# Performance work log

Hardware: AMD Instinct MI355X
Metric: run time of the kernel (lower is better)

## Reference

```python
import jax, jax.numpy as jnp
import numpy as np

BG_W = 1.0
DILATED_BG_W = 5.0
EDGE_W = 20.0
KSIZE = 3


def setup_inputs() -> dict:
    key = jax.random.key(0)
    k1, k2 = jax.random.split(key)
    B, C, H, W = 16, 1, 1024, 1024
    pred = jax.random.normal(k1, (B, C, H, W), dtype=jnp.float32)
    target = (jax.random.uniform(k2, (B, C, H, W)) < 0.05).astype(jnp.float32)
    return {"pred": pred, "target": target}


def _dilate(target):
    # cv2.dilate with KSIZExKSIZE rect kernel == max pool, stride 1, SAME padding
    return jax.lax.reduce_window(
        target, -jnp.inf, jax.lax.max,
        window_dimensions=(1, 1, KSIZE, KSIZE),
        window_strides=(1, 1, 1, 1),
        padding="SAME",
    )


def reference(pred, target):
    dilated = _dilate(target)
    # weight: edge pixels (target>0.5) -> EDGE_W, else dilated band -> DILATED_BG_W, else BG_W
    weight = jnp.where(target > 0.5, EDGE_W,
                       jnp.where(dilated > 0.5, DILATED_BG_W, BG_W))
    # binary_cross_entropy_with_logits, reduction='none', then mean
    x = pred
    losses = weight * (jnp.maximum(x, 0.0) - x * target + jnp.log1p(jnp.exp(-jnp.abs(x))))
    return jnp.mean(losses)
```

## Files before the change

kernel.cpp:

```cpp
#include <hip/hip_runtime.h>

#define HH 1024
#define WW 1024
#define BAND 16
#define NT 256

typedef __attribute__((ext_vector_type(4))) float f32x4;

__device__ __forceinline__ float fmax3(float a, float b, float c) {
    return fmaxf(a, fmaxf(b, c));
}

__device__ __forceinline__ float loss_elem(float x, float t, float dil) {
    float w = fmaf(15.0f, t, fmaf(4.0f, dil, 1.0f));
    float a  = fabsf(x);
    float sp = __logf(1.0f + __expf(-a));
    return w * (fmaxf(x, 0.0f) - x * t + sp);
}

template <bool PER_WAVE>
__global__ __launch_bounds__(NT)
__attribute__((amdgpu_waves_per_eu(2, 2)))
void dilatedweightBCE_main(
        const float* __restrict__ pred,
        const float* __restrict__ target,
        float* __restrict__ partial) {
    __shared__ float swave[NT / 64];
    __shared__ float ldsL[NT / 64][BAND];
    __shared__ float ldsR[NT / 64][BAND];

    const int t    = threadIdx.x;
    const int lane = t & 63;
    const int wv   = t >> 6;
    const int c    = t * 4;

    const int l    = blockIdx.x;
    const int xcd  = l & 7;
    const int j    = l >> 3;
    const int img  = j >> 3;
    const int slab = j & 7;
    const int h0   = (xcd * 8 + slab) * BAND;

    const float* timg = target + (size_t)img * HH * WW;
    const float* pimg = pred   + (size_t)img * HH * WW;
    const f32x4 zero = (f32x4)(0.0f);

    f32x4 tr[BAND + 2];
    tr[0] = (h0 > 0)
          ? __builtin_nontemporal_load((const f32x4*)(timg + (size_t)(h0 - 1) * WW + c))
          : zero;
    #pragma unroll
    for (int r = 0; r < BAND; ++r)
        tr[r + 1] = __builtin_nontemporal_load(
            (const f32x4*)(timg + (size_t)(h0 + r) * WW + c));
    tr[BAND + 1] = (h0 + BAND < HH)
          ? __builtin_nontemporal_load((const f32x4*)(timg + (size_t)(h0 + BAND) * WW + c))
          : zero;

    f32x4 xr[BAND];
    #pragma unroll
    for (int r = 0; r < BAND; ++r)
        xr[r] = __builtin_nontemporal_load(
            (const f32x4*)(pimg + (size_t)(h0 + r) * WW + c));

    if (lane == 0) {
        #pragma unroll
        for (int r = 0; r < BAND; ++r)
            ldsL[wv][r] = fmax3(tr[r].x, tr[r + 1].x, tr[r + 2].x);
    }
    if (lane == 63) {
        #pragma unroll
        for (int r = 0; r < BAND; ++r)
            ldsR[wv][r] = fmax3(tr[r].w, tr[r + 1].w, tr[r + 2].w);
    }
    __syncthreads();

    float s = 0.0f;
    #pragma unroll
    for (int r = 0; r < BAND; ++r) {
        f32x4 a = tr[r], m = tr[r + 1], d = tr[r + 2];
        float vmx = fmax3(a.x, m.x, d.x);
        float vmy = fmax3(a.y, m.y, d.y);
        float vmz = fmax3(a.z, m.z, d.z);
        float vmw = fmax3(a.w, m.w, d.w);

        float lft = __shfl_up(vmw, 1);
        float rgt = __shfl_down(vmx, 1);
        if (lane == 0)  lft = (wv > 0)            ? ldsR[wv - 1][r] : 0.0f;
        if (lane == 63) rgt = (wv < NT / 64 - 1)  ? ldsL[wv + 1][r] : 0.0f;

        float d0 = fmax3(lft, vmx, vmy);
        float d1 = fmax3(vmx, vmy, vmz);
        float d2 = fmax3(vmy, vmz, vmw);
        float d3 = fmax3(vmz, vmw, rgt);

        f32x4 x = xr[r];
        s += loss_elem(x.x, m.x, d0);
        s += loss_elem(x.y, m.y, d1);
        s += loss_elem(x.z, m.z, d2);
        s += loss_elem(x.w, m.w, d3);
    }

    #pragma unroll
    for (int off = 32; off > 0; off >>= 1)
        s += __shfl_down(s, off);

    if (PER_WAVE) {
        if (lane == 0)
            partial[(size_t)l * (NT / 64) + wv] = s;
    } else {
        if (lane == 0) swave[wv] = s;
        __syncthreads();
        if (t == 0) {
            float tot = 0.0f;
            #pragma unroll
            for (int i = 0; i < NT / 64; ++i) tot += swave[i];
            partial[l] = tot;
        }
    }
}

__global__ __launch_bounds__(1024) void dilatedweightBCE_reduce(
        const float* __restrict__ partial,
        float* __restrict__ out,
        int npart4,
        float inv_n) {
    __shared__ float swave[16];
    const int t = threadIdx.x;

    float s = 0.0f;
    const float4* p4 = (const float4*)partial;
    for (int i = t; i < npart4; i += 1024) {
        float4 v = p4[i];
        s += v.x + v.y + v.z + v.w;
    }

    #pragma unroll
    for (int off = 32; off > 0; off >>= 1)
        s += __shfl_down(s, off);

    const int lane = t & 63;
    if (lane == 0) swave[t >> 6] = s;
    __syncthreads();
    if (t == 0) {
        float tot = 0.0f;
        #pragma unroll
        for (int i = 0; i < 16; ++i) tot += swave[i];
        out[0] = tot * inv_n;
    }
}

extern "C" void kernel_launch(void* const* d_in, const int* in_sizes, int n_in,
                              void* d_out, int out_size, void* d_ws, size_t ws_size,
                              hipStream_t stream) {
    const float* pred   = (const float*)d_in[0];
    const float* target = (const float*)d_in[1];
    float* out     = (float*)d_out;
    float* partial = (float*)d_ws;

    const int n  = in_sizes[0];
    const int Bn = n / (HH * WW);
    const int nblocks = (HH / BAND) * Bn;

    const size_t need = (size_t)nblocks * (NT / 64) * sizeof(float);
    if (ws_size >= need) {
        dilatedweightBCE_main<true><<<nblocks, NT, 0, stream>>>(pred, target, partial);
        dilatedweightBCE_reduce<<<1, 1024, 0, stream>>>(partial, out,
                                                        nblocks * (NT / 64) / 4,
                                                        1.0f / (float)n);
    } else {
        dilatedweightBCE_main<false><<<nblocks, NT, 0, stream>>>(pred, target, partial);
        dilatedweightBCE_reduce<<<1, 1024, 0, stream>>>(partial, out,
                                                        nblocks / 4,
                                                        1.0f / (float)n);
    }
}
```

Baseline: 140.0 us.

## Fuse main and reduce kernels via cooperative launch with grid sync

Replaces the two-kernel sequence (per-slab partial sums, then a single-block reduce) with one cooperative kernel that writes per-block partials, performs a grid-wide sync, and has block 0 compute the final mean. The aim is to remove the second kernel launch and its inter-kernel gap. It requires all 1024 blocks to be co-resident, so occupancy is raised to 4 waves per EU. The grid-sync barrier adds its own cost, and a fallback to the old path is kept in case the cooperative launch fails.

```diff
diff --git a/kernel.cpp b/kernel.cpp
--- a/kernel.cpp
+++ b/kernel.cpp
@@ -1,9 +1,13 @@
 #include <hip/hip_runtime.h>
+#include <hip/hip_cooperative_groups.h>
+
+namespace cg = cooperative_groups;
 
 #define HH 1024
 #define WW 1024
 #define BAND 16
 #define NT 256
+#define NBLK ((HH / BAND) * 16)
 
 typedef __attribute__((ext_vector_type(4))) float f32x4;
 
@@ -16,6 +20,112 @@
     float a  = fabsf(x);
     float sp = __logf(1.0f + __expf(-a));
     return w * (fmaxf(x, 0.0f) - x * t + sp);
+}
+
+__global__ __launch_bounds__(NT)
+__attribute__((amdgpu_waves_per_eu(4, 4)))
+void dilatedweightBCE_fused(
+        const float* __restrict__ pred,
+        const float* __restrict__ target,
+        float* __restrict__ partial,
+        float* __restrict__ out,
+        float inv_n) {
+    __shared__ float swave[NT / 64];
+    __shared__ float ldsL[NT / 64][BAND];
+    __shared__ float ldsR[NT / 64][BAND];
+
+    const int t    = threadIdx.x;
+    const int lane = t & 63;
+    const int wv   = t >> 6;
+    const int c    = t * 4;
+
+    const int l    = blockIdx.x;
+    const int xcd  = l & 7;
+    const int j    = l >> 3;
+    const int img  = j >> 3;
+    const int slab = j & 7;
+    const int h0   = (xcd * 8 + slab) * BAND;
+
+    const float* timg = target + (size_t)img * HH * WW;
+    const float* pimg = pred   + (size_t)img * HH * WW;
+    const f32x4 zero = (f32x4)(0.0f);
+
+    f32x4 tr[BAND + 2];
+    tr[0] = (h0 > 0)
+          ? __builtin_nontemporal_load((const f32x4*)(timg + (size_t)(h0 - 1) * WW + c))
+          : zero;
+    #pragma unroll
+    for (int r = 0; r < BAND; ++r)
+        tr[r + 1] = __builtin_nontemporal_load(
+            (const f32x4*)(timg + (size_t)(h0 + r) * WW + c));
+    tr[BAND + 1] = (h0 + BAND < HH)
+          ? __builtin_nontemporal_load((const f32x4*)(timg + (size_t)(h0 + BAND) * WW + c))
+          : zero;
+
+    f32x4 xr[BAND];
+    #pragma unroll
+    for (int r = 0; r < BAND; ++r)
+        xr[r] = __builtin_nontemporal_load(
+            (const f32x4*)(pimg + (size_t)(h0 + r) * WW + c));
+
+    if (lane == 0) {
+        #pragma unroll
+        for (int r = 0; r < BAND; ++r)
+            ldsL[wv][r] = fmax3(tr[r].x, tr[r + 1].x, tr[r + 2].x);
+    }
+    if (lane == 63) {
+        #pragma unroll
+        for (int r = 0; r < BAND; ++r)
+            ldsR[wv][r] = fmax3(tr[r].w, tr[r + 1].w, tr[r + 2].w);
+    }
+    __syncthreads();
+
+    float s = 0.0f;
+    #pragma unroll
+    for (int r = 0; r < BAND; ++r) {
+        f32x4 a = tr[r], m = tr[r + 1], d = tr[r + 2];
+        float vmx = fmax3(a.x, m.x, d.x);
+        float vmy = fmax3(a.y, m.y, d.y);
+        float vmz = fmax3(a.z, m.z, d.z);
+        float vmw = fmax3(a.w, m.w, d.w);
+
+        float lft = __shfl_up(vmw, 1);
+        float rgt = __shfl_down(vmx, 1);
+        if (lane == 0)  lft = (wv > 0)            ? ldsR[wv - 1][r] : 0.0f;
+        if (lane == 63) rgt = (wv < NT / 64 - 1)  ? ldsL[wv + 1][r] : 0.0f;
+
+        float d0 = fmax3(lft, vmx, vmy);
+        float d1 = fmax3(vmx, vmy, vmz);
+        float d2 = fmax3(vmy, vmz, vmw);
+        float d3 = fmax3(vmz, vmw, rgt);
+
+        f32x4 x = xr[r];
+        s += loss_elem(x.x, m.x, d0);
+        s += loss_elem(x.y, m.y, d1);
+        s += loss_elem(x.z, m.z, d2);
+        s += loss_elem(x.w, m.w, d3);
+    }
+
+    #pragma unroll
+    for (int off = 32; off > 0; off >>= 1)
+        s += __shfl_down(s, off);
+    if (lane == 0) swave[wv] = s;
+    __syncthreads();
+    if (t == 0)
+        partial[l] = swave[0] + swave[1] + swave[2] + swave[3];
+
+    cg::this_grid().sync();
+
+    if (l == 0) {
+        float v = partial[t] + partial[t + 256] + partial[t + 512] + partial[t + 768];
+        #pragma unroll
+        for (int off = 32; off > 0; off >>= 1)
+            v += __shfl_down(v, off);
+        if (lane == 0) swave[wv] = v;
+        __syncthreads();
+        if (t == 0)
+            out[0] = (swave[0] + swave[1] + swave[2] + swave[3]) * inv_n;
+    }
 }
 
 template <bool PER_WAVE>
@@ -86,8 +196,8 @@
 
         float lft = __shfl_up(vmw, 1);
         float rgt = __shfl_down(vmx, 1);
-        if (lane == 0)  lft = (wv > 0)            ? ldsR[wv - 1][r] : 0.0f;
-        if (lane == 63) rgt = (wv < NT / 64 - 1)  ? ldsL[wv + 1][r] : 0.0f;
+        if (lane == 0)  lft = (wv > 0)           ? ldsR[wv - 1][r] : 0.0f;
+        if (lane == 63) rgt = (wv < NT / 64 - 1) ? ldsL[wv + 1][r] : 0.0f;
 
         float d0 = fmax3(lft, vmx, vmy);
         float d1 = fmax3(vmx, vmy, vmz);
@@ -159,19 +269,28 @@
     float* partial = (float*)d_ws;
 
     const int n  = in_sizes[0];
-    const int Bn = n / (HH * WW);
-    const int nblocks = (HH / BAND) * Bn;
-
-    const size_t need = (size_t)nblocks * (NT / 64) * sizeof(float);
-    if (ws_size >= need) {
-        dilatedweightBCE_main<true><<<nblocks, NT, 0, stream>>>(pred, target, partial);
-        dilatedweightBCE_reduce<<<1, 1024, 0, stream>>>(partial, out,
-                                                        nblocks * (NT / 64) / 4,
-                                                        1.0f / (float)n);
-    } else {
-        dilatedweightBCE_main<false><<<nblocks, NT, 0, stream>>>(pred, target, partial);
-        dilatedweightBCE_reduce<<<1, 1024, 0, stream>>>(partial, out,
-                                                        nblocks / 4,
-                                                        1.0f / (float)n);
-    }
-}
+    float inv_n  = 1.0f / (float)n;
+
+    void* kargs[] = { (void*)&pred, (void*)&target, (void*)&partial,
+                      (void*)&out, (void*)&inv_n };
+    hipError_t err = hipLaunchCooperativeKernel(
+        (const void*)dilatedweightBCE_fused,
+        dim3(NBLK), dim3(NT), kargs, 0, stream);
+
+    if (err != hipSuccess) {
+        const int Bn = n / (HH * WW);
+        const int nblocks = (HH / BAND) * Bn;
+        const size_t need = (size_t)nblocks * (NT / 64) * sizeof(float);
+        if (ws_size >= need) {
+            dilatedweightBCE_main<true><<<nblocks, NT, 0, stream>>>(pred, target, partial);
+            dilatedweightBCE_reduce<<<1, 1024, 0, stream>>>(partial, out,
+                                                            nblocks * (NT / 64) / 4,
+                                                            inv_n);
+        } else {
+            dilatedweightBCE_main<false><<<nblocks, NT, 0, stream>>>(pred, target, partial);
+            dilatedweightBCE_reduce<<<1, 1024, 0, stream>>>(partial, out,
+                                                            nblocks / 4,
+                                                            inv_n);
+        }
+    }
+}
```

After: 317.2 us. +126.6%, slower.
